# Optimization experiments

Hardware: AMD Instinct MI355X
Metric: run time of the kernel (lower is better)

Reference implementation:

```python
import jax, jax.numpy as jnp
import numpy as np

N = 100000      # nodes
E = 1600000     # edges (avg degree 16)
F_IN = 256
F_OUT = 128


def setup_inputs() -> dict:
    key = jax.random.key(0)
    k1, k2, k3, k4, k5 = jax.random.split(key, 5)
    x = jax.random.normal(k1, (N, F_IN), dtype=jnp.float32)
    adj_row = jax.random.randint(k2, (E,), 0, N, dtype=jnp.int32)
    adj_col = jax.random.randint(k3, (E,), 0, N, dtype=jnp.int32)
    adj_vals = jax.random.uniform(k4, (E,), dtype=jnp.float32)
    # he_uniform init for weight, zeros for bias (as in build())
    limit = jnp.sqrt(6.0 / F_IN)
    w = jax.random.uniform(k5, (F_IN, F_OUT), minval=-limit, maxval=limit, dtype=jnp.float32)
    b = jnp.zeros((F_OUT,), dtype=jnp.float32)
    return {"x": x, "adj_row": adj_row, "adj_col": adj_col, "adj_vals": adj_vals, "w": w, "b": b}


def reference(x, adj_row, adj_col, adj_vals, w, b):
    # dense feature transform: [N, F_in] @ [F_in, F_out] -> [N, F_out]
    h = x @ w
    # sparse adjacency SpMM (COO): out[r] += vals[e] * h[c] for edge e=(r,c)
    msgs = adj_vals[:, None] * h[adj_col]            # [E, F_out]
    agg = jax.ops.segment_sum(msgs, adj_row, num_segments=N)  # [N, F_out]
    # bias + relu activation
    return jax.nn.relu(agg + b)
```

## Files before the change

kernel.cpp:

```cpp
#include <hip/hip_runtime.h>
#include <hip/hip_bf16.h>
#include <cstdint>
#include <cstddef>

#define N_NODES 100000
#define N_EDGES 1600000
#define F_IN 256
#define F_OUT 128

#define NB 782
#define NBLK 196
#define TILE 8192
#define CAP 4096

typedef __attribute__((ext_vector_type(8))) short short8;
typedef __attribute__((ext_vector_type(4))) float floatx4;

static __device__ __forceinline__ unsigned short f2bf(float f) {
    union { float f; unsigned u; } v; v.f = f;
    unsigned r = v.u + 0x7FFF + ((v.u >> 16) & 1);
    return (unsigned short)(r >> 16);
}

__global__ void prep_w(const float* __restrict__ w, unsigned short* __restrict__ wT) {
    int i = blockIdx.x * 256 + threadIdx.x;
    int k = i >> 7;
    int n = i & 127;
    int g = (k >> 3) ^ (n & 7);
    wT[n * 256 + g * 8 + (k & 7)] = f2bf(w[i]);
}

__global__ __launch_bounds__(256, 2) void gemm_xw(const float* __restrict__ x,
                                                  const unsigned short* __restrict__ wT,
                                                  unsigned short* __restrict__ h) {
    __shared__ __align__(16) unsigned short wlds[128 * 256];
    const int tid = threadIdx.x;
    {
        const floatx4* src = reinterpret_cast<const floatx4*>(wT);
        floatx4* dst = reinterpret_cast<floatx4*>(wlds);
        #pragma unroll
        for (int i = 0; i < 16; i++) dst[tid + i * 256] = src[tid + i * 256];
    }
    __syncthreads();

    const int wave = tid >> 6, lane = tid & 63;
    const int quad = lane >> 4, l16 = lane & 15;
    const int rowbase = blockIdx.x * 256 + wave * 64;

    floatx4 acc[4][8];
    #pragma unroll
    for (int mf = 0; mf < 4; mf++)
        #pragma unroll
        for (int nt = 0; nt < 8; nt++) acc[mf][nt] = (floatx4)0.f;

    #pragma unroll
    for (int ks = 0; ks < 8; ks++) {
        const int k0 = ks * 32 + quad * 8;
        short8 afrag[4];
        #pragma unroll
        for (int mf = 0; mf < 4; mf++) {
            int row = rowbase + mf * 16 + l16;
            if (row >= N_NODES) row = N_NODES - 1;
            const float* xp = x + (size_t)row * F_IN + k0;
            floatx4 x0 = *reinterpret_cast<const floatx4*>(xp);
            floatx4 x1 = *reinterpret_cast<const floatx4*>(xp + 4);
            short8 a;
            a[0] = (short)f2bf(x0[0]); a[1] = (short)f2bf(x0[1]);
            a[2] = (short)f2bf(x0[2]); a[3] = (short)f2bf(x0[3]);
            a[4] = (short)f2bf(x1[0]); a[5] = (short)f2bf(x1[1]);
            a[6] = (short)f2bf(x1[2]); a[7] = (short)f2bf(x1[3]);
            afrag[mf] = a;
        }
        short8 bfrag[8];
        const int gq = ks * 4 + quad;
        #pragma unroll
        for (int nt = 0; nt < 8; nt++) {
            const int n = nt * 16 + l16;
            const int g = gq ^ (n & 7);
            bfrag[nt] = *reinterpret_cast<const short8*>(&wlds[n * 256 + g * 8]);
        }
        #pragma unroll
        for (int mf = 0; mf < 4; mf++)
            #pragma unroll
            for (int nt = 0; nt < 8; nt++)
                acc[mf][nt] = __builtin_amdgcn_mfma_f32_16x16x32_bf16(
                    afrag[mf], bfrag[nt], acc[mf][nt], 0, 0, 0);
    }

    #pragma unroll
    for (int mf = 0; mf < 4; mf++) {
        const int mbase = rowbase + mf * 16 + quad * 4;
        #pragma unroll
        for (int reg = 0; reg < 4; reg++) {
            const int m = mbase + reg;
            if (m < N_NODES) {
                #pragma unroll
                for (int nt = 0; nt < 8; nt++)
                    h[(size_t)m * F_OUT + nt * 16 + l16] = f2bf(acc[mf][nt][reg]);
            }
        }
    }
}

__global__ __launch_bounds__(256) void bucket_hist(const int* __restrict__ row,
                                                   int* __restrict__ bucket_total,
                                                   int* __restrict__ blockbase) {
    __shared__ int hist[NB];
    const int t = threadIdx.x, blk = blockIdx.x;
    for (int i = t; i < NB; i += 256) hist[i] = 0;
    __syncthreads();
    const long tb = (long)blk * TILE;
    #pragma unroll
    for (int c = 0; c < 8; c++) {
        long i0 = tb + c * 1024 + t * 4;
        if (i0 + 4 <= N_EDGES) {
            int4 r = *reinterpret_cast<const int4*>(row + i0);
            atomicAdd(&hist[r.x >> 7], 1); atomicAdd(&hist[r.y >> 7], 1);
            atomicAdd(&hist[r.z >> 7], 1); atomicAdd(&hist[r.w >> 7], 1);
        } else {
            for (long i = i0; i < N_EDGES && i < i0 + 4; i++)
                atomicAdd(&hist[row[i] >> 7], 1);
        }
    }
    __syncthreads();
    for (int bin = t; bin < NB; bin += 256)
        blockbase[bin * NBLK + blk] = atomicAdd(&bucket_total[bin], hist[bin]);
}

__global__ void bucket_scan(const int* __restrict__ bucket_total,
                            int* __restrict__ bucket_base) {
    __shared__ int sm[1024];
    const int t = threadIdx.x;
    int v = (t < NB) ? bucket_total[t] : 0;
    sm[t] = v; __syncthreads();
    for (int off = 1; off < 1024; off <<= 1) {
        int x2 = (t >= off) ? sm[t - off] : 0;
        __syncthreads();
        sm[t] += x2;
        __syncthreads();
    }
    if (t < NB) bucket_base[t] = sm[t] - v;
    if (t == NB - 1) bucket_base[NB] = sm[t];
}

__global__ __launch_bounds__(256) void bucket_scatter(const int* __restrict__ row,
                                                      const int* __restrict__ col,
                                                      const float* __restrict__ val,
                                                      const int* __restrict__ bucket_base,
                                                      const int* __restrict__ blockbase,
                                                      int2* __restrict__ metabuf) {
    __shared__ int sbase[NB];
    const int t = threadIdx.x, blk = blockIdx.x;
    for (int bin = t; bin < NB; bin += 256)
        sbase[bin] = bucket_base[bin] + blockbase[bin * NBLK + blk];
    __syncthreads();
    const long tb = (long)blk * TILE;
    #pragma unroll
    for (int c = 0; c < 8; c++) {
        long i0 = tb + c * 1024 + t * 4;
        if (i0 + 4 <= N_EDGES) {
            int4 r  = *reinterpret_cast<const int4*>(row + i0);
            int4 cc = *reinterpret_cast<const int4*>(col + i0);
            floatx4 vv = *reinterpret_cast<const floatx4*>(val + i0);
            int rr[4] = {r.x, r.y, r.z, r.w};
            int c4[4] = {cc.x, cc.y, cc.z, cc.w};
            float v4[4] = {vv[0], vv[1], vv[2], vv[3]};
            #pragma unroll
            for (int j = 0; j < 4; j++) {
                int bin = rr[j] >> 7, rl = rr[j] & 127;
                int pos = atomicAdd(&sbase[bin], 1);
                metabuf[pos] = make_int2(c4[j] | (rl << 24), __float_as_int(v4[j]));
            }
        } else {
            for (long i = i0; i < N_EDGES && i < i0 + 4; i++) {
                int rv = row[i];
                int bin = rv >> 7, rl = rv & 127;
                int pos = atomicAdd(&sbase[bin], 1);
                metabuf[pos] = make_int2(col[i] | (rl << 24), __float_as_int(val[i]));
            }
        }
    }
}

__global__ __launch_bounds__(256) void bucket_bin(const int* __restrict__ bucket_base,
                                                  int2* __restrict__ metabuf,
                                                  int* __restrict__ cnt,
                                                  int* __restrict__ row_start) {
    __shared__ int2 st[CAP];
    __shared__ int hist[128], scanb[128], cursor[128];
    const int t = threadIdx.x, b = blockIdx.x;
    const int b0 = bucket_base[b], e = bucket_base[b + 1];
    int n = e - b0; if (n > CAP) n = CAP;
    if (t < 128) hist[t] = 0;
    __syncthreads();
    for (int i = t; i < n; i += 256) {
        int2 w = metabuf[b0 + i];
        st[i] = w;
        atomicAdd(&hist[((unsigned)w.x >> 24) & 127], 1);
    }
    __syncthreads();
    if (t < 128) scanb[t] = hist[t];
    __syncthreads();
    for (int off = 1; off < 128; off <<= 1) {
        int v = (t >= off && t < 128) ? scanb[t - off] : 0;
        __syncthreads();
        if (t < 128) scanb[t] += v;
        __syncthreads();
    }
    if (t < 128) {
        int excl = scanb[t] - hist[t];
        cursor[t] = excl;
        int r = b * 128 + t;
        if (r < N_NODES) { cnt[r] = hist[t]; row_start[r] = b0 + excl; }
    }
    __syncthreads();
    for (int i = t; i < n; i += 256) {
        int2 w = st[i];
        int rl = ((unsigned)w.x >> 24) & 127;
        int pos = atomicAdd(&cursor[rl], 1);
        metabuf[b0 + pos] = make_int2(w.x & 0x00FFFFFF, w.y);
    }
}

__global__ __launch_bounds__(256) void spmm(const unsigned short* __restrict__ h,
                                            const int* __restrict__ row_start,
                                            const int* __restrict__ cnt,
                                            const int2* __restrict__ meta,
                                            const float* __restrict__ bias,
                                            float* __restrict__ out) {
    const int wave = threadIdx.x >> 6, lane = threadIdx.x & 63;
    const int g = lane >> 4, l16 = lane & 15;
    const int r = blockIdx.x * 4 + wave;
    if (r >= N_NODES) return;
    const int start = row_start[r], deg = cnt[r];

    float acc[8];
    #pragma unroll
    for (int d = 0; d < 8; d++) acc[d] = 0.f;

    const unsigned short* hp = h + l16 * 8;

    if (deg > 0) {
        for (int i = 0; i < deg; i += 16) {
            int2 mm[4];
            #pragma unroll
            for (int u = 0; u < 4; u++) {
                int idx = i + u * 4 + g;
                if (idx > deg - 1) idx = deg - 1;
                mm[u] = meta[start + idx];
            }
            uint4 hv[4];
            #pragma unroll
            for (int u = 0; u < 4; u++)
                hv[u] = *reinterpret_cast<const uint4*>(hp + (size_t)mm[u].x * F_OUT);
            #pragma unroll
            for (int u = 0; u < 4; u++) {
                float v = (i + u * 4 + g < deg) ? __int_as_float(mm[u].y) : 0.f;
                #pragma unroll
                for (int d = 0; d < 4; d++) {
                    unsigned uu = ((const unsigned*)&hv[u])[d];
                    acc[2 * d]     += v * __uint_as_float(uu << 16);
                    acc[2 * d + 1] += v * __uint_as_float(uu & 0xffff0000u);
                }
            }
        }
    }

    #pragma unroll
    for (int d = 0; d < 8; d++) {
        acc[d] += __shfl_xor(acc[d], 16);
        acc[d] += __shfl_xor(acc[d], 32);
    }
    float s0 = (g & 1) ? acc[2] : acc[0];
    float s1 = (g & 1) ? acc[3] : acc[1];
    float t0 = (g & 1) ? acc[6] : acc[4];
    float t1 = (g & 1) ? acc[7] : acc[5];
    float o0 = (g & 2) ? t0 : s0;
    float o1 = (g & 2) ? t1 : s1;
    const int ch = l16 * 8 + g * 2;
    o0 = fmaxf(o0 + bias[ch], 0.f);
    o1 = fmaxf(o1 + bias[ch + 1], 0.f);
    float2 o; o.x = o0; o.y = o1;
    *reinterpret_cast<float2*>(out + (size_t)r * F_OUT + ch) = o;
}

extern "C" void kernel_launch(void* const* d_in, const int* in_sizes, int n_in,
                              void* d_out, int out_size, void* d_ws, size_t ws_size,
                              hipStream_t stream) {
    const float* x        = (const float*)d_in[0];
    const int*   adj_row  = (const int*)d_in[1];
    const int*   adj_col  = (const int*)d_in[2];
    const float* adj_vals = (const float*)d_in[3];
    const float* w        = (const float*)d_in[4];
    const float* b        = (const float*)d_in[5];
    float* out = (float*)d_out;

    char* ws = (char*)d_ws;
    unsigned short* wT = (unsigned short*)ws;
    unsigned short* h  = (unsigned short*)(ws + 65536);
    size_t off = 65536 + (size_t)N_NODES * F_OUT * 2;
    int2* metabuf  = (int2*)(ws + off);   off += (size_t)N_EDGES * 8;
    int* cnt       = (int*)(ws + off);    off += (size_t)N_NODES * 4;
    int* row_start = (int*)(ws + off);    off += (size_t)N_NODES * 4;
    int* blockbase = (int*)(ws + off);    off += (size_t)NB * NBLK * 4;
    int* bucket_total = (int*)(ws + off); off += 3136;
    int* bucket_base  = (int*)(ws + off); off += 3136;

    prep_w<<<128, 256, 0, stream>>>(w, wT);
    hipMemsetAsync(bucket_total, 0, NB * 4, stream);
    gemm_xw<<<(N_NODES + 255) / 256, 256, 0, stream>>>(x, wT, h);
    bucket_hist<<<NBLK, 256, 0, stream>>>(adj_row, bucket_total, blockbase);
    bucket_scan<<<1, 1024, 0, stream>>>(bucket_total, bucket_base);
    bucket_scatter<<<NBLK, 256, 0, stream>>>(adj_row, adj_col, adj_vals,
                                             bucket_base, blockbase, metabuf);
    bucket_bin<<<NB, 256, 0, stream>>>(bucket_base, metabuf, cnt, row_start);
    spmm<<<N_NODES / 4, 256, 0, stream>>>(h, row_start, cnt, metabuf, b, out);
}
```

Baseline: 310.6 us.

## Pad CSR rows to multiples of eight and process two rows per wave in SpMM

Builds a padded CSR in a new buffer, with each row's edge list rounded up to a multiple of eight with zero entries and a packed (start, iterations) descriptor per row. The SpMM kernel then runs without bounds checks and handles two rows per wave, using a single shuffle reduction and float4 stores. The GEMM drops the LDS staging of W in favour of direct global loads of a re-laid-out weight array with smaller 128-row tiles, and the bucket counter memset is folded into prep_w. Padding adds extra gathers of row zero and an extra global atomic allocation, and because csr_pad blocks claim space through an atomic, the row layout order is not deterministic.

```diff
diff --git a/kernel.cpp b/kernel.cpp
--- a/kernel.cpp
+++ b/kernel.cpp
@@ -12,6 +12,7 @@
 #define NBLK 196
 #define TILE 8192
 #define CAP 4096
+#define META2_CAP 2400000
 
 typedef __attribute__((ext_vector_type(8))) short short8;
 typedef __attribute__((ext_vector_type(4))) float floatx4;
@@ -22,43 +23,35 @@
     return (unsigned short)(r >> 16);
 }
 
-__global__ void prep_w(const float* __restrict__ w, unsigned short* __restrict__ wT) {
+__global__ void prep_w(const float* __restrict__ w, unsigned short* __restrict__ wT2,
+                       int* __restrict__ bucket_total) {
     int i = blockIdx.x * 256 + threadIdx.x;
+    if (i <= NB) bucket_total[i] = 0;
     int k = i >> 7;
     int n = i & 127;
-    int g = (k >> 3) ^ (n & 7);
-    wT[n * 256 + g * 8 + (k & 7)] = f2bf(w[i]);
-}
-
-__global__ __launch_bounds__(256, 2) void gemm_xw(const float* __restrict__ x,
-                                                  const unsigned short* __restrict__ wT,
-                                                  unsigned short* __restrict__ h) {
-    __shared__ __align__(16) unsigned short wlds[128 * 256];
+    wT2[(k >> 3) * 1024 + n * 8 + (k & 7)] = f2bf(w[i]);
+}
+
+__global__ __launch_bounds__(256) void gemm_xw(const float* __restrict__ x,
+                                               const unsigned short* __restrict__ wT2,
+                                               unsigned short* __restrict__ h) {
     const int tid = threadIdx.x;
-    {
-        const floatx4* src = reinterpret_cast<const floatx4*>(wT);
-        floatx4* dst = reinterpret_cast<floatx4*>(wlds);
-        #pragma unroll
-        for (int i = 0; i < 16; i++) dst[tid + i * 256] = src[tid + i * 256];
-    }
-    __syncthreads();
-
     const int wave = tid >> 6, lane = tid & 63;
     const int quad = lane >> 4, l16 = lane & 15;
-    const int rowbase = blockIdx.x * 256 + wave * 64;
-
-    floatx4 acc[4][8];
-    #pragma unroll
-    for (int mf = 0; mf < 4; mf++)
+    const int rowbase = blockIdx.x * 128 + wave * 32;
+
+    floatx4 acc[2][8];
+    #pragma unroll
+    for (int mf = 0; mf < 2; mf++)
         #pragma unroll
         for (int nt = 0; nt < 8; nt++) acc[mf][nt] = (floatx4)0.f;
 
     #pragma unroll
     for (int ks = 0; ks < 8; ks++) {
         const int k0 = ks * 32 + quad * 8;
-        short8 afrag[4];
-        #pragma unroll
-        for (int mf = 0; mf < 4; mf++) {
+        short8 afrag[2];
+        #pragma unroll
+        for (int mf = 0; mf < 2; mf++) {
             int row = rowbase + mf * 16 + l16;
             if (row >= N_NODES) row = N_NODES - 1;
             const float* xp = x + (size_t)row * F_IN + k0;
@@ -72,15 +65,12 @@
             afrag[mf] = a;
         }
         short8 bfrag[8];
-        const int gq = ks * 4 + quad;
-        #pragma unroll
-        for (int nt = 0; nt < 8; nt++) {
-            const int n = nt * 16 + l16;
-            const int g = gq ^ (n & 7);
-            bfrag[nt] = *reinterpret_cast<const short8*>(&wlds[n * 256 + g * 8]);
-        }
-        #pragma unroll
-        for (int mf = 0; mf < 4; mf++)
+        const unsigned short* bp = wT2 + (size_t)(ks * 4 + quad) * 1024 + l16 * 8;
+        #pragma unroll
+        for (int nt = 0; nt < 8; nt++)
+            bfrag[nt] = *reinterpret_cast<const short8*>(bp + nt * 128);
+        #pragma unroll
+        for (int mf = 0; mf < 2; mf++)
             #pragma unroll
             for (int nt = 0; nt < 8; nt++)
                 acc[mf][nt] = __builtin_amdgcn_mfma_f32_16x16x32_bf16(
@@ -88,7 +78,7 @@
     }
 
     #pragma unroll
-    for (int mf = 0; mf < 4; mf++) {
+    for (int mf = 0; mf < 2; mf++) {
         const int mbase = rowbase + mf * 16 + quad * 4;
         #pragma unroll
         for (int reg = 0; reg < 4; reg++) {
@@ -182,12 +172,14 @@
     }
 }
 
-__global__ __launch_bounds__(256) void bucket_bin(const int* __restrict__ bucket_base,
-                                                  int2* __restrict__ metabuf,
-                                                  int* __restrict__ cnt,
-                                                  int* __restrict__ row_start) {
+__global__ __launch_bounds__(256) void csr_pad(const int* __restrict__ bucket_base,
+                                               const int2* __restrict__ metabuf,
+                                               int* __restrict__ alloc,
+                                               int2* __restrict__ meta2,
+                                               int2* __restrict__ row_desc) {
     __shared__ int2 st[CAP];
     __shared__ int hist[128], scanb[128], cursor[128];
+    __shared__ int sbase_sh;
     const int t = threadIdx.x, b = blockIdx.x;
     const int b0 = bucket_base[b], e = bucket_base[b + 1];
     int n = e - b0; if (n > CAP) n = CAP;
@@ -199,7 +191,7 @@
         atomicAdd(&hist[((unsigned)w.x >> 24) & 127], 1);
     }
     __syncthreads();
-    if (t < 128) scanb[t] = hist[t];
+    if (t < 128) scanb[t] = (hist[t] + 7) & ~7;
     __syncthreads();
     for (int off = 1; off < 128; off <<= 1) {
         int v = (t >= off && t < 128) ? scanb[t - off] : 0;
@@ -207,81 +199,75 @@
         if (t < 128) scanb[t] += v;
         __syncthreads();
     }
+    if (t == 127) sbase_sh = atomicAdd(alloc, scanb[127]);
+    __syncthreads();
     if (t < 128) {
-        int excl = scanb[t] - hist[t];
-        cursor[t] = excl;
+        int c = hist[t], p = (c + 7) & ~7;
+        int base_row = sbase_sh + scanb[t] - p;
+        cursor[t] = base_row;
         int r = b * 128 + t;
-        if (r < N_NODES) { cnt[r] = hist[t]; row_start[r] = b0 + excl; }
+        if (r < N_NODES) row_desc[r] = make_int2(base_row, p >> 3);
+        for (int k = c; k < p; k++) meta2[base_row + k] = make_int2(0, 0);
     }
     __syncthreads();
     for (int i = t; i < n; i += 256) {
         int2 w = st[i];
         int rl = ((unsigned)w.x >> 24) & 127;
         int pos = atomicAdd(&cursor[rl], 1);
-        metabuf[b0 + pos] = make_int2(w.x & 0x00FFFFFF, w.y);
+        meta2[pos] = make_int2(w.x & 0x00FFFFFF, w.y);
     }
 }
 
 __global__ __launch_bounds__(256) void spmm(const unsigned short* __restrict__ h,
-                                            const int* __restrict__ row_start,
-                                            const int* __restrict__ cnt,
+                                            const int2* __restrict__ row_desc,
                                             const int2* __restrict__ meta,
                                             const float* __restrict__ bias,
                                             float* __restrict__ out) {
     const int wave = threadIdx.x >> 6, lane = threadIdx.x & 63;
     const int g = lane >> 4, l16 = lane & 15;
-    const int r = blockIdx.x * 4 + wave;
-    if (r >= N_NODES) return;
-    const int start = row_start[r], deg = cnt[r];
+    const int gi = g & 1;
+    const int r = blockIdx.x * 8 + wave * 2 + (g >> 1);
+    const int2 d = row_desc[r];
+    const int start = d.x, niter = d.y;
 
     float acc[8];
     #pragma unroll
-    for (int d = 0; d < 8; d++) acc[d] = 0.f;
+    for (int k = 0; k < 8; k++) acc[k] = 0.f;
 
     const unsigned short* hp = h + l16 * 8;
-
-    if (deg > 0) {
-        for (int i = 0; i < deg; i += 16) {
-            int2 mm[4];
+    const int2* mp = meta + start + gi * 4;
+
+    for (int it = 0; it < niter; ++it) {
+        int2 mm[4];
+        #pragma unroll
+        for (int u = 0; u < 4; u++) mm[u] = mp[it * 8 + u];
+        uint4 hv[4];
+        #pragma unroll
+        for (int u = 0; u < 4; u++)
+            hv[u] = *reinterpret_cast<const uint4*>(hp + (size_t)mm[u].x * F_OUT);
+        #pragma unroll
+        for (int u = 0; u < 4; u++) {
+            float v = __int_as_float(mm[u].y);
             #pragma unroll
-            for (int u = 0; u < 4; u++) {
-                int idx = i + u * 4 + g;
-                if (idx > deg - 1) idx = deg - 1;
-                mm[u] = meta[start + idx];
+            for (int dd = 0; dd < 4; dd++) {
+                unsigned uu = ((const unsigned*)&hv[u])[dd];
+                acc[2 * dd]     += v * __uint_as_float(uu << 16);
+                acc[2 * dd + 1] += v * __uint_as_float(uu & 0xffff0000u);
             }
-            uint4 hv[4];
-            #pragma unroll
-            for (int u = 0; u < 4; u++)
-                hv[u] = *reinterpret_cast<const uint4*>(hp + (size_t)mm[u].x * F_OUT);
-            #pragma unroll
-            for (int u = 0; u < 4; u++) {
-                float v = (i + u * 4 + g < deg) ? __int_as_float(mm[u].y) : 0.f;
-                #pragma unroll
-                for (int d = 0; d < 4; d++) {
-                    unsigned uu = ((const unsigned*)&hv[u])[d];
-                    acc[2 * d]     += v * __uint_as_float(uu << 16);
-                    acc[2 * d + 1] += v * __uint_as_float(uu & 0xffff0000u);
-                }
-            }
-        }
-    }
-
-    #pragma unroll
-    for (int d = 0; d < 8; d++) {
-        acc[d] += __shfl_xor(acc[d], 16);
-        acc[d] += __shfl_xor(acc[d], 32);
-    }
-    float s0 = (g & 1) ? acc[2] : acc[0];
-    float s1 = (g & 1) ? acc[3] : acc[1];
-    float t0 = (g & 1) ? acc[6] : acc[4];
-    float t1 = (g & 1) ? acc[7] : acc[5];
-    float o0 = (g & 2) ? t0 : s0;
-    float o1 = (g & 2) ? t1 : s1;
-    const int ch = l16 * 8 + g * 2;
-    o0 = fmaxf(o0 + bias[ch], 0.f);
-    o1 = fmaxf(o1 + bias[ch + 1], 0.f);
-    float2 o; o.x = o0; o.y = o1;
-    *reinterpret_cast<float2*>(out + (size_t)r * F_OUT + ch) = o;
+        }
+    }
+
+    #pragma unroll
+    for (int k = 0; k < 8; k++) acc[k] += __shfl_xor(acc[k], 16);
+
+    const int ch = l16 * 8 + gi * 4;
+    float4 bv = *reinterpret_cast<const float4*>(bias + ch);
+    float o0 = fmaxf((gi ? acc[4] : acc[0]) + bv.x, 0.f);
+    float o1 = fmaxf((gi ? acc[5] : acc[1]) + bv.y, 0.f);
+    float o2 = fmaxf((gi ? acc[6] : acc[2]) + bv.z, 0.f);
+    float o3 = fmaxf((gi ? acc[7] : acc[3]) + bv.w, 0.f);
+    float4 o; o.x = o0; o.y = o1; o.z = o2; o.w = o3;
+    *reinterpret_cast<float4*>(out + (size_t)r * F_OUT + ch) = o;
 }
 
 extern "C" void kernel_launch(void* const* d_in, const int* in_sizes, int n_in,
@@ -296,23 +282,23 @@
     float* out = (float*)d_out;
 
     char* ws = (char*)d_ws;
-    unsigned short* wT = (unsigned short*)ws;
-    unsigned short* h  = (unsigned short*)(ws + 65536);
+    unsigned short* wT2 = (unsigned short*)ws;
+    unsigned short* h   = (unsigned short*)(ws + 65536);
     size_t off = 65536 + (size_t)N_NODES * F_OUT * 2;
     int2* metabuf  = (int2*)(ws + off);   off += (size_t)N_EDGES * 8;
-    int* cnt       = (int*)(ws + off);    off += (size_t)N_NODES * 4;
-    int* row_start = (int*)(ws + off);    off += (size_t)N_NODES * 4;
+    int2* meta2    = (int2*)(ws + off);   off += (size_t)META2_CAP * 8;
+    int2* row_desc = (int2*)(ws + off);   off += (size_t)100096 * 8;
     int* blockbase = (int*)(ws + off);    off += (size_t)NB * NBLK * 4;
-    int* bucket_total = (int*)(ws + off); off += 3136;
-    int* bucket_base  = (int*)(ws + off); off += 3136;
-
-    prep_w<<<128, 256, 0, stream>>>(w, wT);
-    hipMemsetAsync(bucket_total, 0, NB * 4, stream);
-    gemm_xw<<<(N_NODES + 255) / 256, 256, 0, stream>>>(x, wT, h);
+    int* bucket_total = (int*)(ws + off); off += 4096;
+    int* bucket_base  = (int*)(ws + off); off += 4096;
+
+    prep_w<<<128, 256, 0, stream>>>(w, wT2, bucket_total);
+    gemm_xw<<<782, 256, 0, stream>>>(x, wT2, h);
     bucket_hist<<<NBLK, 256, 0, stream>>>(adj_row, bucket_total, blockbase);
     bucket_scan<<<1, 1024, 0, stream>>>(bucket_total, bucket_base);
     bucket_scatter<<<NBLK, 256, 0, stream>>>(adj_row, adj_col, adj_vals,
                                              bucket_base, blockbase, metabuf);
-    bucket_bin<<<NB, 256, 0, stream>>>(bucket_base, metabuf, cnt, row_start);
-    spmm<<<N_NODES / 4, 256, 0, stream>>>(h, row_start, cnt, metabuf, b, out);
-}
+    csr_pad<<<NB, 256, 0, stream>>>(bucket_base, metabuf, bucket_total + NB,
+                                    meta2, row_desc);
+    spmm<<<12500, 256, 0, stream>>>(h, row_desc, meta2, b, out);
+}
```

Result: slower. 322.3 us (+3.8%).
